# Performance work log

Measured on AMD Instinct MI355X. Metric: run time of the kernel, lower is better.

Reference implementation:

```python
import jax, jax.numpy as jnp
import numpy as np

DIM = 512
HEADS = 8
DIM_HEAD = 64
INNER = HEADS * DIM_HEAD  # 512
BN_EPS = 1e-5


def _bn(x, gamma, beta, mean, var):
    # BatchNorm1d in eval mode over channel axis 1 of [b, c, n]
    inv = gamma / jnp.sqrt(var + BN_EPS)
    return x * inv[None, :, None] + (beta - mean * inv)[None, :, None]


def setup_inputs() -> dict:
    key = jax.random.key(0)
    ks = jax.random.split(key, 12)
    b, d, n = 4, DIM, 2048
    s = 0.02
    return {
        "x": jax.random.normal(ks[0], (b, d, n), dtype=jnp.float32),
        "W_qkv": jax.random.normal(ks[1], (3 * INNER, DIM), dtype=jnp.float32) * s,
        "W_out": jax.random.normal(ks[2], (DIM, INNER), dtype=jnp.float32) * s,
        "b_out": jax.random.normal(ks[3], (DIM,), dtype=jnp.float32) * s,
        "g1": jax.random.normal(ks[4], (DIM,), dtype=jnp.float32) * 0.1 + 1.0,
        "beta1": jax.random.normal(ks[5], (DIM,), dtype=jnp.float32) * 0.1,
        "m1": jax.random.normal(ks[6], (DIM,), dtype=jnp.float32) * 0.1,
        "v1": jax.random.uniform(ks[7], (DIM,), minval=0.5, maxval=1.5, dtype=jnp.float32),
        "W_ffn": jax.random.normal(ks[8], (DIM, DIM), dtype=jnp.float32) * s,
        "g2": jax.random.normal(ks[9], (DIM,), dtype=jnp.float32) * 0.1 + 1.0,
        "beta2": jax.random.normal(ks[10], (DIM,), dtype=jnp.float32) * 0.1,
        "m2": jax.random.normal(ks[11], (DIM,), dtype=jnp.float32) * 0.1,
        "v2": jax.random.uniform(jax.random.fold_in(key, 99), (DIM,), minval=0.5, maxval=1.5, dtype=jnp.float32),
    }


def reference(x, W_qkv, W_out, b_out, g1, beta1, m1, v1, W_ffn, g2, beta2, m2, v2):
    b, d, n = x.shape
    h, dh = HEADS, DIM_HEAD
    scale = dh ** -0.5

    # ---- Attention (manual QKV + einsum softmax attention) ----
    xt = jnp.einsum("bdn->bnd", x)                       # [b, n, d]
    qkv = xt @ W_qkv.T                                   # [b, n, 3*inner]
    q, k, v = jnp.split(qkv, 3, axis=-1)
    def to_heads(t):
        return t.reshape(b, n, h, dh).transpose(0, 2, 1, 3)  # [b, h, n, dh]
    q, k, v = to_heads(q), to_heads(k), to_heads(v)
    dots = jnp.einsum("bhid,bhjd->bhij", q, k) * scale   # [b, h, n, n]
    attn = jax.nn.softmax(dots, axis=-1)
    out = jnp.einsum("bhij,bhjd->bhid", attn, v)         # [b, h, n, dh]
    out = out.transpose(0, 2, 1, 3).reshape(b, n, h * dh).transpose(0, 2, 1)  # [b, inner, n]
    # to_out: Conv1d(inner, dim, 1, bias=True) + BatchNorm1d(dim)
    out = jnp.einsum("oc,bcn->bon", W_out, out) + b_out[None, :, None]
    att_out = _bn(out, g1, beta1, m1, v1)

    # ---- Residual + GELU, then FFN (Conv1d 1x1 no bias + BN), residual + GELU ----
    att = jax.nn.gelu(att_out + x, approximate=False)
    ffn = _bn(jnp.einsum("oc,bcn->bon", W_ffn, att), g2, beta2, m2, v2)
    return jax.nn.gelu(att + ffn, approximate=False)
```

## Files before the change

kernel.cpp:

```cpp
#include <hip/hip_runtime.h>
#include <math.h>

#define N_TOK 2048

typedef __attribute__((ext_vector_type(8))) short short8;
typedef __attribute__((ext_vector_type(4))) float f32x4;

__device__ __forceinline__ float gelu_f(float v) {
    return 0.5f * v * (1.0f + erff(v * 0.7071067811865475f));
}
__device__ __forceinline__ ushort f2bf(float x) {
    uint u = __float_as_uint(x);
    uint r = u + 0x7FFFu + ((u >> 16) & 1u);
    return (ushort)(r >> 16);
}
__device__ __forceinline__ float bf2f(ushort u) {
    return __uint_as_float((uint)u << 16);
}
__device__ __forceinline__ void gload16(const void* g, void* s) {
    __builtin_amdgcn_global_load_lds((const __attribute__((address_space(1))) void*)g,
                                     (__attribute__((address_space(3))) void*)s, 16, 0, 0);
}

__global__ __launch_bounds__(256)
void prep(const float* __restrict__ w0, ushort* __restrict__ o0,
          const float* __restrict__ w1, ushort* __restrict__ o1,
          const float* __restrict__ w2, ushort* __restrict__ o2,
          const float* __restrict__ x, ushort* __restrict__ xt)
{
    __shared__ ushort sT[64 * 68];
    const int tid = threadIdx.x;
    int bx = blockIdx.x;
    if (bx < 1280) {
        int i4 = bx * 256 + tid;
        const float* src; ushort* dst; int idx;
        if (i4 < 196608)      { src = w0; dst = o0; idx = i4; }
        else if (i4 < 262144) { src = w1; dst = o1; idx = i4 - 196608; }
        else                  { src = w2; dst = o2; idx = i4 - 262144; }
        float4 v = *(const float4*)&src[idx * 4];
        ushort4 p; p.x = f2bf(v.x); p.y = f2bf(v.y); p.z = f2bf(v.z); p.w = f2bf(v.w);
        *(ushort4*)&dst[idx * 4] = p;
        return;
    }
    bx -= 1280;
    const int tok0 = (bx & 31) * 64;
    const int ch0 = ((bx >> 5) & 7) * 64;
    const int bi = bx >> 8;
    #pragma unroll
    for (int i = 0; i < 4; i++) {
        int ch = (tid >> 4) + i * 16;
        int t4 = (tid & 15) * 4;
        float4 v = *(const float4*)&x[((size_t)bi * 512 + ch0 + ch) * N_TOK + tok0 + t4];
        ushort4 p; p.x = f2bf(v.x); p.y = f2bf(v.y); p.z = f2bf(v.z); p.w = f2bf(v.w);
        *(ushort4*)&sT[ch * 68 + t4] = p;
    }
    __syncthreads();
    const int tr = (tid & 15) + (tid >> 6) * 16;
    const int cb = ((tid >> 4) & 3) * 16;
    uint vv[8];
    #pragma unroll
    for (int j = 0; j < 8; j++) {
        uint lo = sT[(cb + 2 * j) * 68 + tr];
        uint hi = sT[(cb + 2 * j + 1) * 68 + tr];
        vv[j] = lo | (hi << 16);
    }
    size_t base = ((size_t)bi * N_TOK + tok0 + tr) * 512 + ch0 + cb;
    *(uint4*)&xt[base]     = *(uint4*)&vv[0];
    *(uint4*)&xt[base + 8] = *(uint4*)&vv[4];
}

template<int MODE, int BM, int BN>
__global__ __launch_bounds__(256)
void bgemm(const ushort* __restrict__ A, const ushort* __restrict__ Bt, int M,
           ushort* __restrict__ qt, ushort* __restrict__ vc,
           float* __restrict__ outF, ushort* __restrict__ outB,
           const float* __restrict__ bias,
           const float* __restrict__ g, const float* __restrict__ be,
           const float* __restrict__ mu, const float* __restrict__ va,
           const ushort* __restrict__ residB)
{
    constexpr int MF = BM / 32, NF = BN / 32;
    __shared__ ushort sA[BM * 64];
    __shared__ ushort sB[BN * 64];
    const int tid = threadIdx.x;
    const int w = tid >> 6, l = tid & 63;
    const int l16 = l & 15, lg = l >> 4;
    const int wr = w >> 1, wc = w & 1;
    const int bi = blockIdx.z;
    const int m0 = blockIdx.y * BM, n0 = blockIdx.x * BN;
    const ushort* Bb = Bt + (size_t)bi * N_TOK * 512;
    const int srow = l >> 3, spos = l & 7;

    f32x4 acc[MF][NF];
    #pragma unroll
    for (int i = 0; i < MF; i++)
        #pragma unroll
        for (int j = 0; j < NF; j++) acc[i][j] = (f32x4){0.f, 0.f, 0.f, 0.f};

    for (int kt = 0; kt < 512; kt += 64) {
        __syncthreads();
        #pragma unroll
        for (int i = 0; i < BM / 32; i++) {
            int row = w * (BM / 4) + i * 8 + srow;
            int c = spos ^ (row & 7);
            gload16(A + (size_t)(m0 + row) * 512 + kt + c * 8,
                    sA + (w * (BM / 4) + i * 8) * 64);
        }
        #pragma unroll
        for (int i = 0; i < BN / 32; i++) {
            int row = w * (BN / 4) + i * 8 + srow;
            int c = spos ^ (row & 7);
            gload16(Bb + (size_t)(n0 + row) * 512 + kt + c * 8,
                    sB + (w * (BN / 4) + i * 8) * 64);
        }
        __syncthreads();
        #pragma unroll
        for (int ks = 0; ks < 2; ks++) {
            short8 af[MF], bfv[NF];
            #pragma unroll
            for (int mi = 0; mi < MF; mi++) {
                int row = wr * (BM / 2) + mi * 16 + l16;
                af[mi] = *(const short8*)&sA[row * 64 + (((ks * 4 + lg) ^ (row & 7)) << 3)];
            }
            #pragma unroll
            for (int ni = 0; ni < NF; ni++) {
                int row = wc * (BN / 2) + ni * 16 + l16;
                bfv[ni] = *(const short8*)&sB[row * 64 + (((ks * 4 + lg) ^ (row & 7)) << 3)];
            }
            __builtin_amdgcn_s_setprio(1);
            #pragma unroll
            for (int mi = 0; mi < MF; mi++)
                #pragma unroll
                for (int ni = 0; ni < NF; ni++)
                    acc[mi][ni] = __builtin_amdgcn_mfma_f32_16x16x32_bf16(
                        af[mi], bfv[ni], acc[mi][ni], 0, 0, 0);
            __builtin_amdgcn_s_setprio(0);
        }
    }

    const int chb = m0 + wr * (BM / 2);
    const int tkb = n0 + wc * (BN / 2);
    if (MODE == 0) {
        if (m0 < 1024) {
            const float qs = (m0 < 512) ? 0.18033688f : 1.0f;
            #pragma unroll
            for (int mi = 0; mi < MF; mi++) {
                int ob = chb + mi * 16 + lg * 4;
                #pragma unroll
                for (int ni = 0; ni < NF; ni++) {
                    int tok = tkb + ni * 16 + l16;
                    ushort4 p;
                    p.x = f2bf(acc[mi][ni][0] * qs); p.y = f2bf(acc[mi][ni][1] * qs);
                    p.z = f2bf(acc[mi][ni][2] * qs); p.w = f2bf(acc[mi][ni][3] * qs);
                    *(ushort4*)&qt[((size_t)bi * N_TOK + tok) * 1024 + ob] = p;
                }
            }
        } else {
            #pragma unroll
            for (int mi = 0; mi < MF; mi++)
                #pragma unroll
                for (int r = 0; r < 4; r++) {
                    int o = chb + mi * 16 + lg * 4 + r - 1024;
                    #pragma unroll
                    for (int ni = 0; ni < NF; ni++) {
                        int tok = tkb + ni * 16 + l16;
                        vc[((size_t)bi * 512 + o) * N_TOK + tok] = f2bf(acc[mi][ni][r]);
                    }
                }
        }
    } else {
        #pragma unroll
        for (int mi = 0; mi < MF; mi++) {
            float inv[4], sh[4], bb[4];
            #pragma unroll
            for (int r = 0; r < 4; r++) {
                int o = chb + mi * 16 + lg * 4 + r;
                inv[r] = g[o] * rsqrtf(va[o] + 1e-5f);
                sh[r]  = be[o] - mu[o] * inv[r];
                bb[r]  = (MODE == 1) ? bias[o] : 0.f;
            }
            #pragma unroll
            for (int ni = 0; ni < NF; ni++) {
                int tok = tkb + ni * 16 + l16;
                ushort4 rv = *(const ushort4*)&residB[((size_t)bi * N_TOK + tok) * 512 +
                                                      chb + mi * 16 + lg * 4];
                float rr_[4] = {bf2f(rv.x), bf2f(rv.y), bf2f(rv.z), bf2f(rv.w)};
                float ov[4];
                #pragma unroll
                for (int r = 0; r < 4; r++) {
                    float y = (acc[mi][ni][r] + bb[r]) * inv[r] + sh[r];
                    ov[r] = gelu_f((MODE == 1) ? (y + rr_[r]) : (rr_[r] + y));
                }
                if (MODE == 1) {
                    ushort4 p;
                    p.x = f2bf(ov[0]); p.y = f2bf(ov[1]);
                    p.z = f2bf(ov[2]); p.w = f2bf(ov[3]);
                    *(ushort4*)&outB[((size_t)bi * N_TOK + tok) * 512 +
                                     chb + mi * 16 + lg * 4] = p;
                } else {
                    #pragma unroll
                    for (int r = 0; r < 4; r++) {
                        int o = chb + mi * 16 + lg * 4 + r;
                        outF[((size_t)bi * 512 + o) * N_TOK + tok] = ov[r];
                    }
                }
            }
        }
    }
}

__global__ __launch_bounds__(256)
void attn_mfma(const ushort* __restrict__ qt, const ushort* __restrict__ vc,
               ushort* __restrict__ aout)
{
    __shared__ ushort sK[2][64 * 64];
    __shared__ ushort sV[2][64 * 64];
    __shared__ uint   sPu[4][1024];
    const int tid = threadIdx.x;
    const int w = tid >> 6, l = tid & 63;
    const int l16 = l & 15, lg = l >> 4;
    const int h = blockIdx.y, bi = blockIdx.z;
    const int qw = blockIdx.x * 128 + w * 32;
    const int srow = l >> 3, spos = l & 7;
    const int swz = (l16 & 7) << 2;
    uint* sPw = &sPu[w][0];

    const ushort* kSrc = qt + (size_t)bi * N_TOK * 1024 + 512 + h * 64 + ((spos ^ srow) << 3);
    const ushort* vSrc = vc + (size_t)(bi * 512 + h * 64) * N_TOK + ((spos ^ srow) << 3);

    short8 qf[2][2];
    #pragma unroll
    for (int Mt = 0; Mt < 2; Mt++)
        #pragma unroll
        for (int kt = 0; kt < 2; kt++)
            qf[Mt][kt] = *(const short8*)(qt +
                ((size_t)(bi * N_TOK + qw + Mt * 16 + l16) * 1024 + h * 64 + kt * 32 + lg * 8));

    f32x4 oacc[2][4];
    #pragma unroll
    for (int Mt = 0; Mt < 2; Mt++)
        #pragma unroll
        for (int dt = 0; dt < 4; dt++) oacc[Mt][dt] = (f32x4){0.f, 0.f, 0.f, 0.f};
    float lsum[2] = {0.f, 0.f};

    #pragma unroll
    for (int i = 0; i < 2; i++) {
        int rk = w * 16 + i * 8;
        gload16(kSrc + (size_t)(rk + srow) * 1024, &sK[0][rk * 64]);
        gload16(vSrc + (size_t)(rk + srow) * N_TOK, &sV[0][rk * 64]);
    }

    for (int t = 0; t < N_TOK / 64; t++) {
        const int cur = t & 1;
        __syncthreads();
        if (t + 1 < N_TOK / 64) {
            const int kv1 = (t + 1) * 64;
            #pragma unroll
            for (int i = 0; i < 2; i++) {
                int rk = w * 16 + i * 8;
                gload16(kSrc + (size_t)(kv1 + rk + srow) * 1024, &sK[cur ^ 1][rk * 64]);
                gload16(vSrc + (size_t)(rk + srow) * N_TOK + kv1, &sV[cur ^ 1][rk * 64]);
            }
        }

        f32x4 sacc[2][4];
        #pragma unroll
        for (int Mt = 0; Mt < 2; Mt++)
            #pragma unroll
            for (int nt = 0; nt < 4; nt++) sacc[Mt][nt] = (f32x4){0.f, 0.f, 0.f, 0.f};
        __builtin_amdgcn_s_setprio(1);
        #pragma unroll
        for (int nt = 0; nt < 4; nt++)
            #pragma unroll
            for (int kt = 0; kt < 2; kt++) {
                short8 kf = *(const short8*)&sK[cur][(nt * 16 + l16) * 64 +
                                                     (((kt * 4 + lg) ^ (l16 & 7)) << 3)];
                #pragma unroll
                for (int Mt = 0; Mt < 2; Mt++)
                    sacc[Mt][nt] = __builtin_amdgcn_mfma_f32_16x16x32_bf16(
                        kf, qf[Mt][kt], sacc[Mt][nt], 0, 0, 0);
            }
        __builtin_amdgcn_s_setprio(0);

        #pragma unroll
        for (int Mt = 0; Mt < 2; Mt++) {
            float ps = 0.f;
            #pragma unroll
            for (int nt = 0; nt < 4; nt++)
                #pragma unroll
                for (int r = 0; r < 4; r++) {
                    float p = __builtin_amdgcn_exp2f(sacc[Mt][nt][r]);
                    sacc[Mt][nt][r] = p;
                    ps += p;
                }
            ps += __shfl_xor(ps, 16);
            ps += __shfl_xor(ps, 32);
            lsum[Mt] += ps;
            #pragma unroll
            for (int nt = 0; nt < 4; nt++) {
                float a0 = sacc[Mt][nt][0], a1 = sacc[Mt][nt][1];
                float a2 = sacc[Mt][nt][2], a3 = sacc[Mt][nt][3];
                uint u0, u1;
                asm("v_cvt_pk_bf16_f32 %0, %1, %2" : "=v"(u0) : "v"(a0), "v"(a1));
                asm("v_cvt_pk_bf16_f32 %0, %1, %2" : "=v"(u1) : "v"(a2), "v"(a3));
                int col = ((nt * 4 + lg) * 2) ^ swz;
                *(uint2*)&sPw[Mt * 512 + l16 * 32 + col] = make_uint2(u0, u1);
            }
        }

        #pragma unroll
        for (int kt = 0; kt < 2; kt++) {
            short8 pf[2];
            #pragma unroll
            for (int Mt = 0; Mt < 2; Mt++)
                pf[Mt] = *(const short8*)&sPw[Mt * 512 + l16 * 32 +
                                              ((kt * 16 + lg * 4) ^ swz)];
            __builtin_amdgcn_s_setprio(1);
            #pragma unroll
            for (int dt = 0; dt < 4; dt++) {
                short8 vf = *(const short8*)&sV[cur][(dt * 16 + l16) * 64 +
                                                     (((kt * 4 + lg) ^ (l16 & 7)) << 3)];
                #pragma unroll
                for (int Mt = 0; Mt < 2; Mt++)
                    oacc[Mt][dt] = __builtin_amdgcn_mfma_f32_16x16x32_bf16(
                        pf[Mt], vf, oacc[Mt][dt], 0, 0, 0);
            }
            __builtin_amdgcn_s_setprio(0);
        }
    }

    #pragma unroll
    for (int Mt = 0; Mt < 2; Mt++) {
        float rl = 1.f / lsum[Mt];
        float rr[4];
        #pragma unroll
        for (int r = 0; r < 4; r++) rr[r] = __shfl(rl, lg * 4 + r);
        #pragma unroll
        for (int dt = 0; dt < 4; dt++) {
            int ch = h * 64 + dt * 16 + l16;
            #pragma unroll
            for (int r = 0; r < 4; r++) {
                int tok = qw + Mt * 16 + lg * 4 + r;
                aout[((size_t)bi * N_TOK + tok) * 512 + ch] = f2bf(oacc[Mt][dt][r] * rr[r]);
            }
        }
    }
}

extern "C" void kernel_launch(void* const* d_in, const int* in_sizes, int n_in,
                              void* d_out, int out_size, void* d_ws, size_t ws_size,
                              hipStream_t stream) {
    const float* x    = (const float*)d_in[0];
    const float* Wqkv = (const float*)d_in[1];
    const float* Wout = (const float*)d_in[2];
    const float* bout = (const float*)d_in[3];
    const float* g1   = (const float*)d_in[4];
    const float* be1  = (const float*)d_in[5];
    const float* m1   = (const float*)d_in[6];
    const float* v1   = (const float*)d_in[7];
    const float* Wffn = (const float*)d_in[8];
    const float* g2   = (const float*)d_in[9];
    const float* be2  = (const float*)d_in[10];
    const float* m2   = (const float*)d_in[11];
    const float* v2   = (const float*)d_in[12];

    char* ws = (char*)d_ws;
    ushort* wqB  = (ushort*)(ws + 0);
    ushort* woB  = (ushort*)(ws + 1572864);
    ushort* wfB  = (ushort*)(ws + 2097152);
    ushort* xt   = (ushort*)(ws + 2621440);
    ushort* qtp  = (ushort*)(ws + 11010048);
    ushort* vcp  = (ushort*)(ws + 27787264);
    ushort* aout = (ushort*)(ws + 36175872);
    ushort* attB = (ushort*)(ws + 27787264);

    dim3 blk(256);
    prep<<<2304, blk, 0, stream>>>(Wqkv, wqB, Wout, woB, Wffn, wfB, x, xt);
    bgemm<0, 128, 128><<<dim3(16, 12, 4), blk, 0, stream>>>(
        wqB, xt, 1536, qtp, vcp, nullptr, nullptr,
        nullptr, nullptr, nullptr, nullptr, nullptr, nullptr);
    attn_mfma<<<dim3(16, 8, 4), blk, 0, stream>>>(qtp, vcp, aout);
    bgemm<1, 64, 128><<<dim3(16, 8, 4), blk, 0, stream>>>(
        woB, aout, 512, nullptr, nullptr, nullptr, attB,
        bout, g1, be1, m1, v1, xt);
    bgemm<2, 64, 128><<<dim3(16, 8, 4), blk, 0, stream>>>(
        wfB, attB, 512, nullptr, nullptr, (float*)d_out, nullptr,
        nullptr, g2, be2, m2, v2, attB);
}
```

Before: 122.7 us.

## Load K/V fragments directly from global in attention and remap blocks for L2 locality

The attention kernel stops staging K and V tiles through double-buffered LDS with async global-to-LDS loads and per-iteration barriers. Each wave now reads its K and V MFMA fragments straight from global memory. The grid is flattened to 1D with a block-index remap, so the blocks that share a (batch, head) K/V stream are spread across XCDs in a way meant to improve L2/cache reuse. This removes the LDS traffic and __syncthreads, but every wave now fetches K/V itself with no explicit prefetch, which depends on cache hits and may expose global latency.

```diff
diff --git a/kernel.cpp b/kernel.cpp
--- a/kernel.cpp
+++ b/kernel.cpp
@@ -213,20 +213,21 @@
 void attn_mfma(const ushort* __restrict__ qt, const ushort* __restrict__ vc,
                ushort* __restrict__ aout)
 {
-    __shared__ ushort sK[2][64 * 64];
-    __shared__ ushort sV[2][64 * 64];
-    __shared__ uint   sPu[4][1024];
+    __shared__ uint sPu[4][1024];
     const int tid = threadIdx.x;
     const int w = tid >> 6, l = tid & 63;
     const int l16 = l & 15, lg = l >> 4;
-    const int h = blockIdx.y, bi = blockIdx.z;
-    const int qw = blockIdx.x * 128 + w * 32;
-    const int srow = l >> 3, spos = l & 7;
+    const int phys = blockIdx.x;
+    const int logi = (phys & 7) * 64 + (phys >> 3);
+    const int qt6 = logi & 15;
+    const int pair = logi >> 4;
+    const int h = pair & 7, bi = pair >> 3;
+    const int qw = qt6 * 128 + w * 32;
     const int swz = (l16 & 7) << 2;
     uint* sPw = &sPu[w][0];
 
-    const ushort* kSrc = qt + (size_t)bi * N_TOK * 1024 + 512 + h * 64 + ((spos ^ srow) << 3);
-    const ushort* vSrc = vc + (size_t)(bi * 512 + h * 64) * N_TOK + ((spos ^ srow) << 3);
+    const ushort* Kb = qt + (size_t)bi * N_TOK * 1024 + 512 + h * 64;
+    const ushort* Vb = vc + (size_t)(bi * 512 + h * 64) * N_TOK;
 
     short8 qf[2][2];
     #pragma unroll
@@ -243,25 +244,16 @@
         for (int dt = 0; dt < 4; dt++) oacc[Mt][dt] = (f32x4){0.f, 0.f, 0.f, 0.f};
     float lsum[2] = {0.f, 0.f};
 
-    #pragma unroll
-    for (int i = 0; i < 2; i++) {
-        int rk = w * 16 + i * 8;
-        gload16(kSrc + (size_t)(rk + srow) * 1024, &sK[0][rk * 64]);
-        gload16(vSrc + (size_t)(rk + srow) * N_TOK, &sV[0][rk * 64]);
-    }
-
     for (int t = 0; t < N_TOK / 64; t++) {
-        const int cur = t & 1;
-        __syncthreads();
-        if (t + 1 < N_TOK / 64) {
-            const int kv1 = (t + 1) * 64;
-            #pragma unroll
-            for (int i = 0; i < 2; i++) {
-                int rk = w * 16 + i * 8;
-                gload16(kSrc + (size_t)(kv1 + rk + srow) * 1024, &sK[cur ^ 1][rk * 64]);
-                gload16(vSrc + (size_t)(rk + srow) * N_TOK + kv1, &sV[cur ^ 1][rk * 64]);
-            }
-        }
+        const int kv0 = t * 64;
+
+        short8 kf[4][2];
+        #pragma unroll
+        for (int nt = 0; nt < 4; nt++)
+            #pragma unroll
+            for (int kt = 0; kt < 2; kt++)
+                kf[nt][kt] = *(const short8*)(Kb +
+                    (size_t)(kv0 + nt * 16 + l16) * 1024 + kt * 32 + lg * 8);
 
         f32x4 sacc[2][4];
         #pragma unroll
@@ -272,14 +264,11 @@
         #pragma unroll
         for (int nt = 0; nt < 4; nt++)
             #pragma unroll
-            for (int kt = 0; kt < 2; kt++) {
-                short8 kf = *(const short8*)&sK[cur][(nt * 16 + l16) * 64 +
-                                                     (((kt * 4 + lg) ^ (l16 & 7)) << 3)];
+            for (int kt = 0; kt < 2; kt++)
                 #pragma unroll
                 for (int Mt = 0; Mt < 2; Mt++)
                     sacc[Mt][nt] = __builtin_amdgcn_mfma_f32_16x16x32_bf16(
-                        kf, qf[Mt][kt], sacc[Mt][nt], 0, 0, 0);
-            }
+                        kf[nt][kt], qf[Mt][kt], sacc[Mt][nt], 0, 0, 0);
         __builtin_amdgcn_s_setprio(0);
 
         #pragma unroll
@@ -318,8 +307,8 @@
             __builtin_amdgcn_s_setprio(1);
             #pragma unroll
             for (int dt = 0; dt < 4; dt++) {
-                short8 vf = *(const short8*)&sV[cur][(dt * 16 + l16) * 64 +
-                                                     (((kt * 4 + lg) ^ (l16 & 7)) << 3)];
+                short8 vf = *(const short8*)(Vb +
+                    (size_t)(dt * 16 + l16) * N_TOK + kv0 + kt * 32 + lg * 8);
                 #pragma unroll
                 for (int Mt = 0; Mt < 2; Mt++)
                     oacc[Mt][dt] = __builtin_amdgcn_mfma_f32_16x16x32_bf16(
@@ -379,7 +368,7 @@
     bgemm<0, 128, 128><<<dim3(16, 12, 4), blk, 0, stream>>>(
         wqB, xt, 1536, qtp, vcp, nullptr, nullptr,
         nullptr, nullptr, nullptr, nullptr, nullptr, nullptr);
-    attn_mfma<<<dim3(16, 8, 4), blk, 0, stream>>>(qtp, vcp, aout);
+    attn_mfma<<<dim3(512), blk, 0, stream>>>(qtp, vcp, aout);
     bgemm<1, 64, 128><<<dim3(16, 8, 4), blk, 0, stream>>>(
         woB, aout, 512, nullptr, nullptr, nullptr, attB,
         bout, g1, be1, m1, v1, xt);
```

New measurement: 180.7 us. 1.47x slower.
